# Optimization experiments

Measured on AMD Instinct MI355X. Metric: run time of the kernel, lower is better.

Reference implementation:

```python
import jax, jax.numpy as jnp
import numpy as np

MIN_VAL = 0.0
MAX_VAL = 1.0
NUM_BINS = 512
NUM_NODES = 128
GRAD_SMOOTH = 0.01
BIN_W = (MAX_VAL - MIN_VAL) / NUM_BINS


def _make_kernels():
    sobel = jnp.array([-1.0, 0.0, 1.0], dtype=jnp.float32) / (2.0 * BIN_W)
    r = max(1, int(GRAD_SMOOTH / BIN_W))  # kernel radius in bins
    idx = jnp.arange(2 * r + 1, dtype=jnp.float32) - r
    sigma = GRAD_SMOOTH / BIN_W
    g = jnp.exp(-0.5 * (idx / sigma) ** 2)
    return sobel, g / jnp.sum(g)


def _conv1d_reflect(x, k):
    # x: [N, B], k: [K]; torch Conv1d = cross-correlation with reflect padding
    pad = (k.shape[0] - 1) // 2
    xp = jnp.pad(x, ((0, 0), (pad, pad)), mode='reflect')
    out = jax.lax.conv_general_dilated(
        xp[:, None, :], k[None, None, :], (1,), 'VALID',
        dimension_numbers=('NCH', 'OIH', 'NCH'))
    return out[:, 0, :]


def _compute_cdf_pdf(residuals, weights, src_indices, dst_indices):
    # histogram bin per sample (floor)
    bi = jnp.floor((residuals - MIN_VAL) / BIN_W).astype(jnp.int32)
    valid = (bi >= 0) & (bi < NUM_BINS)
    bi = jnp.clip(bi, 0, NUM_BINS - 1)
    wc = (weights * valid).reshape(-1)  # [N_pairs*K]

    src_comb = (src_indices[:, None] * NUM_BINS + bi).reshape(-1)
    dst_comb = (dst_indices[:, None] * NUM_BINS + bi).reshape(-1)
    nseg = NUM_NODES * NUM_BINS
    hist = (jax.ops.segment_sum(wc, src_comb, num_segments=nseg)
            + jax.ops.segment_sum(wc, dst_comb, num_segments=nseg))
    hist = hist.reshape(NUM_NODES, NUM_BINS)

    wflat = weights.reshape(-1)
    src_exp = jnp.broadcast_to(src_indices[:, None], residuals.shape).reshape(-1)
    dst_exp = jnp.broadcast_to(dst_indices[:, None], residuals.shape).reshape(-1)
    tw = (jax.ops.segment_sum(wflat, src_exp, num_segments=NUM_NODES)
          + jax.ops.segment_sum(wflat, dst_exp, num_segments=NUM_NODES))

    pmf = hist / (tw[:, None] + 1e-10)
    cdf = jnp.cumsum(pmf, axis=1)
    sobel, gauss = _make_kernels()
    pdf = _conv1d_reflect(_conv1d_reflect(cdf, sobel), gauss)
    return cdf, pdf


def _lookup(residuals, weights, cdf, pdf, src_indices, dst_indices):
    # rounded bin for lookup (floor of x + 0.5)
    bi = jnp.floor((residuals - MIN_VAL) / BIN_W + 0.5).astype(jnp.int32)
    valid = (bi >= 0) & (bi < NUM_BINS) & (weights > 0.0)
    bi = jnp.clip(bi, 0, NUM_BINS - 1)
    src_cdf = cdf[src_indices[:, None], bi]
    dst_cdf = cdf[dst_indices[:, None], bi]
    src_grad = pdf[src_indices[:, None], bi] * weights
    dst_grad = pdf[dst_indices[:, None], bi] * weights
    two = jnp.float32(2.0)
    return (jnp.where(valid, src_cdf, two),
            jnp.where(valid, src_grad, 0.0),
            jnp.where(valid, dst_cdf, two),
            jnp.where(valid, dst_grad, 0.0))


def setup_inputs() -> dict:
    key = jax.random.key(0)
    k1, k2, k3, k4 = jax.random.split(key, 4)
    N_pairs, K = 1024, 16384
    return {
        'residuals': jax.random.uniform(k1, (N_pairs, K), dtype=jnp.float32),
        'weights': jax.random.uniform(k2, (N_pairs, K), dtype=jnp.float32),
        'src_indices': jax.random.randint(k3, (N_pairs,), 0, NUM_NODES),
        'dst_indices': jax.random.randint(k4, (N_pairs,), 0, NUM_NODES),
    }


def reference(residuals, weights, src_indices, dst_indices):
    cdf, pdf = _compute_cdf_pdf(residuals, weights, src_indices, dst_indices)
    src_cdf, _, dst_cdf, _ = _lookup(residuals, weights, cdf, pdf,
                                     src_indices, dst_indices)
    return src_cdf, dst_cdf
```

## Files before the change

kernel.cpp:

```cpp
#include <hip/hip_runtime.h>

#define NUM_BINS  512
#define NUM_NODES 128
#define K_ELEMS   16384
#define N_PAIRS   1024
#define NCOPY     32

typedef float f32x4 __attribute__((ext_vector_type(4)));
typedef float f32x2 __attribute__((ext_vector_type(2)));
typedef unsigned int   u32;
typedef unsigned short u16;

__device__ __forceinline__ void gfadd(float* p, float v) { unsafeAtomicAdd(p, v); }

__global__ __launch_bounds__(256) void zero_ws_kernel(float* __restrict__ ws, int n)
{
    int i = blockIdx.x * 256 + threadIdx.x;
    if (i < n) ws[i] = 0.0f;
}

__global__ __launch_bounds__(1024) void hist_kernel(
    const float* __restrict__ residuals, const float* __restrict__ weights,
    const int* __restrict__ src, const int* __restrict__ dst,
    float* __restrict__ hist, float* __restrict__ tw,
    u16* __restrict__ codes)
{
    __shared__ u32 lh[NUM_BINS * NCOPY];
    __shared__ float swsum[16];
    const int row  = blockIdx.x;
    const int t    = threadIdx.x;
    const int copy = t & 31;

    uint4* lh4 = (uint4*)lh;
    #pragma unroll
    for (int k = 0; k < NUM_BINS * NCOPY / 4 / 1024; ++k) {
        uint4 z; z.x = z.y = z.z = z.w = 0u;
        lh4[t + k * 1024] = z;
    }
    __syncthreads();

    const f32x4* r4 = (const f32x4*)(residuals + (size_t)row * K_ELEMS);
    const f32x4* w4 = (const f32x4*)(weights   + (size_t)row * K_ELEMS);
    ushort4*     c4 = (ushort4*)(codes + (size_t)row * K_ELEMS);

    float wsum = 0.0f;
    #pragma unroll
    for (int it = 0; it < K_ELEMS / 4 / 1024; ++it) {
        f32x4 r = __builtin_nontemporal_load(r4 + (t + it * 1024));
        f32x4 w = __builtin_nontemporal_load(w4 + (t + it * 1024));
        wsum += w[0] + w[1] + w[2] + w[3];
        ushort4 cv;
        u16* cp = (u16*)&cv;
        #pragma unroll
        for (int c = 0; c < 4; ++c) {
            int b = (int)floorf(r[c] * 512.0f);
            if ((unsigned)b < 512u)
                atomicAdd(&lh[b * NCOPY + copy], (u32)fmaf(w[c], 65536.0f, 0.5f));
            int lb = (int)floorf(r[c] * 512.0f + 0.5f);
            cp[c] = (u16)((((unsigned)lb < 512u) & (w[c] > 0.0f)) ? lb : 0xFFFF);
        }
        c4[t + it * 1024] = cv;
    }

    #pragma unroll
    for (int off = 32; off > 0; off >>= 1) wsum += __shfl_down(wsum, off, 64);
    const int wave = t >> 6, lane = t & 63;
    if (lane == 0) swsum[wave] = wsum;
    __syncthreads();

    const int s = src[row], d = dst[row];
    if (t == 0) {
        float tot = 0.0f;
        #pragma unroll
        for (int i = 0; i < 16; ++i) tot += swsum[i];
        gfadd(&tw[s], tot);
        gfadd(&tw[d], tot);
    }

    {
        const int bin  = t >> 1;
        const int half = t & 1;
        u32 tot = 0;
        #pragma unroll
        for (int cc = 0; cc < 16; ++cc)
            tot += lh[bin * NCOPY + (((bin + cc) & 15) | (half << 4))];
        tot += (u32)__shfl_xor((int)tot, 1);
        float v = (float)tot * (1.0f / 65536.0f);
        if (half == 0) gfadd(&hist[s * NUM_BINS + bin], v);
        else           gfadd(&hist[d * NUM_BINS + bin], v);
    }
}

__global__ __launch_bounds__(512) void scan_kernel(float* __restrict__ hist,
                                                   const float* __restrict__ tw)
{
    __shared__ float s[NUM_BINS];
    const int node = blockIdx.x;
    const int t    = threadIdx.x;

    const float denom = tw[node] + 1e-10f;
    s[t] = hist[node * NUM_BINS + t] / denom;
    __syncthreads();

    for (int off = 1; off < NUM_BINS; off <<= 1) {
        float add = (t >= off) ? s[t - off] : 0.0f;
        __syncthreads();
        s[t] += add;
        __syncthreads();
    }
    hist[node * NUM_BINS + t] = s[t];
}

__global__ __launch_bounds__(256) void lookup_code_kernel(
    const u16* __restrict__ codes,
    const int* __restrict__ src, const int* __restrict__ dst,
    const float* __restrict__ cdf,
    float* __restrict__ out_src, float* __restrict__ out_dst)
{
    __shared__ f32x2 sd[NUM_BINS];
    const int CHUNK = K_ELEMS / 4;
    const int row   = blockIdx.x >> 2;
    const int chunk = blockIdx.x & 3;
    const int t     = threadIdx.x;

    const int s = src[row], d = dst[row];
    for (int i = t; i < NUM_BINS; i += 256) {
        f32x2 v;
        v[0] = cdf[s * NUM_BINS + i];
        v[1] = cdf[d * NUM_BINS + i];
        sd[i] = v;
    }
    __syncthreads();

    const size_t base = (size_t)row * K_ELEMS + (size_t)chunk * CHUNK;
    const ushort4* c4 = (const ushort4*)(codes + base);
    f32x4*        os4 = (f32x4*)(out_src + base);
    f32x4*        od4 = (f32x4*)(out_dst + base);

    for (int i = t; i < CHUNK / 4; i += 256) {
        ushort4 c = c4[i];
        f32x4 osv, odv;
        {   f32x2 v = (c.x != 0xFFFF) ? sd[c.x] : (f32x2){2.0f, 2.0f};
            osv[0] = v[0]; odv[0] = v[1]; }
        {   f32x2 v = (c.y != 0xFFFF) ? sd[c.y] : (f32x2){2.0f, 2.0f};
            osv[1] = v[0]; odv[1] = v[1]; }
        {   f32x2 v = (c.z != 0xFFFF) ? sd[c.z] : (f32x2){2.0f, 2.0f};
            osv[2] = v[0]; odv[2] = v[1]; }
        {   f32x2 v = (c.w != 0xFFFF) ? sd[c.w] : (f32x2){2.0f, 2.0f};
            osv[3] = v[0]; odv[3] = v[1]; }
        __builtin_nontemporal_store(osv, os4 + i);
        __builtin_nontemporal_store(odv, od4 + i);
    }
}

extern "C" void kernel_launch(void* const* d_in, const int* in_sizes, int n_in,
                              void* d_out, int out_size, void* d_ws, size_t ws_size,
                              hipStream_t stream)
{
    const float* residuals = (const float*)d_in[0];
    const float* weights   = (const float*)d_in[1];
    const int*   src       = (const int*)d_in[2];
    const int*   dst       = (const int*)d_in[3];

    float* out_src = (float*)d_out;
    float* out_dst = out_src + (size_t)N_PAIRS * K_ELEMS;

    float* hist  = (float*)d_ws;
    float* tw    = hist + NUM_NODES * NUM_BINS;
    u16*   codes = (u16*)((char*)d_ws + (4u << 20));

    const int ws_elems = NUM_NODES * NUM_BINS + NUM_NODES;
    zero_ws_kernel<<<(ws_elems + 255) / 256, 256, 0, stream>>>((float*)d_ws, ws_elems);

    hist_kernel<<<N_PAIRS, 1024, 0, stream>>>(residuals, weights, src, dst,
                                              hist, tw, codes);

    scan_kernel<<<NUM_NODES, NUM_BINS, 0, stream>>>(hist, tw);

    lookup_code_kernel<<<N_PAIRS * 4, 256, 0, stream>>>(codes, src, dst, hist,
                                                        out_src, out_dst);
}
```

Before: 69.20 us.

## Fuse per-node CDF scan into lookup kernel, recomputing scan per row

Result: no change. 68.03 us (-1.7%).

```diff
diff --git a/kernel.cpp b/kernel.cpp
--- a/kernel.cpp
+++ b/kernel.cpp
@@ -91,54 +91,40 @@
     }
 }
 
-__global__ __launch_bounds__(512) void scan_kernel(float* __restrict__ hist,
-                                                   const float* __restrict__ tw)
+__global__ __launch_bounds__(512) void lookup_scan_kernel(
+    const u16* __restrict__ codes,
+    const int* __restrict__ src, const int* __restrict__ dst,
+    const float* __restrict__ hist, const float* __restrict__ tw,
+    float* __restrict__ out_src, float* __restrict__ out_dst)
 {
-    __shared__ float s[NUM_BINS];
-    const int node = blockIdx.x;
-    const int t    = threadIdx.x;
+    __shared__ f32x2 sd[NUM_BINS];
+    const int row = blockIdx.x;
+    const int t   = threadIdx.x;
 
-    const float denom = tw[node] + 1e-10f;
-    s[t] = hist[node * NUM_BINS + t] / denom;
+    const int s = src[row], d = dst[row];
+    {
+        f32x2 v;
+        v[0] = hist[s * NUM_BINS + t] / (tw[s] + 1e-10f);
+        v[1] = hist[d * NUM_BINS + t] / (tw[d] + 1e-10f);
+        sd[t] = v;
+    }
     __syncthreads();
 
     for (int off = 1; off < NUM_BINS; off <<= 1) {
-        float add = (t >= off) ? s[t - off] : 0.0f;
+        f32x2 add = (t >= off) ? sd[t - off] : (f32x2){0.0f, 0.0f};
         __syncthreads();
-        s[t] += add;
+        sd[t] += add;
         __syncthreads();
     }
-    hist[node * NUM_BINS + t] = s[t];
-}
 
-__global__ __launch_bounds__(256) void lookup_code_kernel(
-    const u16* __restrict__ codes,
-    const int* __restrict__ src, const int* __restrict__ dst,
-    const float* __restrict__ cdf,
-    float* __restrict__ out_src, float* __restrict__ out_dst)
-{
-    __shared__ f32x2 sd[NUM_BINS];
-    const int CHUNK = K_ELEMS / 4;
-    const int row   = blockIdx.x >> 2;
-    const int chunk = blockIdx.x & 3;
-    const int t     = threadIdx.x;
-
-    const int s = src[row], d = dst[row];
-    for (int i = t; i < NUM_BINS; i += 256) {
-        f32x2 v;
-        v[0] = cdf[s * NUM_BINS + i];
-        v[1] = cdf[d * NUM_BINS + i];
-        sd[i] = v;
-    }
-    __syncthreads();
-
-    const size_t base = (size_t)row * K_ELEMS + (size_t)chunk * CHUNK;
+    const size_t base = (size_t)row * K_ELEMS;
     const ushort4* c4 = (const ushort4*)(codes + base);
     f32x4*        os4 = (f32x4*)(out_src + base);
     f32x4*        od4 = (f32x4*)(out_dst + base);
 
-    for (int i = t; i < CHUNK / 4; i += 256) {
-        ushort4 c = c4[i];
+    #pragma unroll
+    for (int it = 0; it < K_ELEMS / 4 / 512; ++it) {
+        ushort4 c = c4[t + it * 512];
         f32x4 osv, odv;
         {   f32x2 v = (c.x != 0xFFFF) ? sd[c.x] : (f32x2){2.0f, 2.0f};
             osv[0] = v[0]; odv[0] = v[1]; }
@@ -148,8 +134,8 @@
             osv[2] = v[0]; odv[2] = v[1]; }
         {   f32x2 v = (c.w != 0xFFFF) ? sd[c.w] : (f32x2){2.0f, 2.0f};
             osv[3] = v[0]; odv[3] = v[1]; }
-        __builtin_nontemporal_store(osv, os4 + i);
-        __builtin_nontemporal_store(odv, od4 + i);
+        __builtin_nontemporal_store(osv, os4 + (t + it * 512));
+        __builtin_nontemporal_store(odv, od4 + (t + it * 512));
     }
 }
 
@@ -175,8 +161,6 @@
     hist_kernel<<<N_PAIRS, 1024, 0, stream>>>(residuals, weights, src, dst,
                                               hist, tw, codes);
 
-    scan_kernel<<<NUM_NODES, NUM_BINS, 0, stream>>>(hist, tw);
-
-    lookup_code_kernel<<<N_PAIRS * 4, 256, 0, stream>>>(codes, src, dst, hist,
-                                                        out_src, out_dst);
+    lookup_scan_kernel<<<N_PAIRS, 512, 0, stream>>>(codes, src, dst, hist, tw,
+                                                    out_src, out_dst);
 }
```
